# Optimization experiments

Hardware: AMD Instinct MI355X
Metric: run time of the kernel (lower is better)

## Reference

```python
import jax, jax.numpy as jnp
import numpy as np
import math

D_MODEL = 1024
N_HEADS = 16
FFN_DIM = 4096
B, L = 8, 1024
LN_EPS = 1e-5


def setup_inputs() -> dict:
    key = jax.random.key(0)
    ks = jax.random.split(key, 16)
    s = 1.0 / math.sqrt(D_MODEL)
    sf = 1.0 / math.sqrt(FFN_DIM)
    # weights stored [in, out] (transposed vs torch nn.Linear)
    return {
        "x": jax.random.normal(ks[0], (B, L, D_MODEL), dtype=jnp.float32),
        "Wq": jax.random.normal(ks[1], (D_MODEL, D_MODEL), dtype=jnp.float32) * s,
        "bq": jnp.zeros((D_MODEL,), jnp.float32),
        "Wk": jax.random.normal(ks[2], (D_MODEL, D_MODEL), dtype=jnp.float32) * s,
        "bk": jnp.zeros((D_MODEL,), jnp.float32),
        "Wv": jax.random.normal(ks[3], (D_MODEL, D_MODEL), dtype=jnp.float32) * s,
        "bv": jnp.zeros((D_MODEL,), jnp.float32),
        "Wo": jax.random.normal(ks[4], (D_MODEL, D_MODEL), dtype=jnp.float32) * s,
        "bo": jnp.zeros((D_MODEL,), jnp.float32),
        "W1": jax.random.normal(ks[5], (D_MODEL, FFN_DIM), dtype=jnp.float32) * s,
        "b1": jnp.zeros((FFN_DIM,), jnp.float32),
        "W2": jax.random.normal(ks[6], (FFN_DIM, D_MODEL), dtype=jnp.float32) * sf,
        "b2": jnp.zeros((D_MODEL,), jnp.float32),
        "gamma": jnp.ones((D_MODEL,), jnp.float32),
        "beta": jnp.zeros((D_MODEL,), jnp.float32),
    }


def reference(x, Wq, bq, Wk, bk, Wv, bv, Wo, bo, W1, b1, W2, b2, gamma, beta):
    Bb, Ll, D = x.shape
    H = N_HEADS
    E = D // H
    scale = 1.0 / math.sqrt(E)
    # multi-head attention (dropout is identity in eval)
    q = (x @ Wq + bq).reshape(Bb, Ll, H, E)
    k = (x @ Wk + bk).reshape(Bb, Ll, H, E)
    v = (x @ Wv + bv).reshape(Bb, Ll, H, E)
    scores = jnp.einsum('blhe,bshe->bhls', q, k)  # [B,H,L,L]
    A = jax.nn.softmax(scale * scores, axis=-1)
    ctx = jnp.einsum('bhls,bshd->blhd', A, v).reshape(Bb, Ll, D)
    attn_out = ctx @ Wo + bo
    x = x + attn_out
    # FFN: conv1d kernel_size=1 == pointwise linear; exact (erf) GELU as in F.gelu
    h = jax.nn.gelu(x @ W1 + b1, approximate=False)
    x = x + (h @ W2 + b2)
    # LayerNorm
    mu = jnp.mean(x, axis=-1, keepdims=True)
    var = jnp.mean(jnp.square(x - mu), axis=-1, keepdims=True)
    out = (x - mu) * jax.lax.rsqrt(var + LN_EPS) * gamma + beta
    return out
```

## Files before the change

### kernel.cpp

```cpp
#include <hip/hip_runtime.h>
#include <cmath>

typedef __attribute__((ext_vector_type(8))) _Float16 half8;
typedef __attribute__((ext_vector_type(4))) _Float16 half4;
typedef __attribute__((ext_vector_type(4))) float f32x4;

__device__ __forceinline__ void glds16(const void* g, void* l) {
  __builtin_amdgcn_global_load_lds(
      (__attribute__((address_space(1))) const void*)g,
      (__attribute__((address_space(3))) void*)l, 16, 0, 0);
}

__device__ __forceinline__ float fast_erf(float x) {
  float ax = fabsf(x);
  float t = 1.0f / (1.0f + 0.3275911f * ax);
  float y = t * (0.254829592f +
            t * (-0.284496736f +
            t * (1.421413741f +
            t * (-1.453152027f + t * 1.061405429f))));
  float r = 1.0f - y * __expf(-ax * ax);
  return copysignf(r, x);
}

__global__ __launch_bounds__(256) void k_cvt(const float* __restrict__ in,
                                             _Float16* __restrict__ out) {
  int i = (blockIdx.x * 256 + threadIdx.x) * 8;
  const f32x4* p = (const f32x4*)(in + i);
  f32x4 a = p[0], b = p[1];
  half8 h;
  h[0] = (_Float16)a[0]; h[1] = (_Float16)a[1]; h[2] = (_Float16)a[2]; h[3] = (_Float16)a[3];
  h[4] = (_Float16)b[0]; h[5] = (_Float16)b[1]; h[6] = (_Float16)b[2]; h[7] = (_Float16)b[3];
  *(half8*)(out + i) = h;
}

__global__ __launch_bounds__(256) void k_wt(const float* __restrict__ W,
                                            _Float16* __restrict__ Wt, int K, int N) {
  __shared__ float t[32][33];
  int x = threadIdx.x & 31, y4 = (threadIdx.x >> 5) << 2;
  int n0 = blockIdx.x << 5, k0 = blockIdx.y << 5;
#pragma unroll
  for (int r = 0; r < 4; ++r) t[y4 + r][x] = W[(size_t)(k0 + y4 + r) * N + n0 + x];
  __syncthreads();
#pragma unroll
  for (int r = 0; r < 4; ++r) Wt[(size_t)(n0 + y4 + r) * K + k0 + x] = (_Float16)t[x][y4 + r];
}

__global__ void k_biascat(const float* __restrict__ a, const float* __restrict__ b,
                          const float* __restrict__ c, float* __restrict__ o) {
  int i = blockIdx.x * 256 + threadIdx.x;
  const float* s = i < 1024 ? a : (i < 2048 ? b : c);
  o[i] = s[i & 1023];
}

template <int BM, int EPI>
__global__ __launch_bounds__(512, 2) void k_gemm8(
    const _Float16* __restrict__ A, const _Float16* __restrict__ Bt,
    const float* __restrict__ bias, const float* __restrict__ res,
    float* __restrict__ outf, _Float16* __restrict__ outh, int M, int N, int K) {
  constexpr int MR = BM / 32;
  constexpr int MH2 = MR / 2;
  constexpr int AL = BM * 64;
  constexpr int BL = 256 * 64;
  constexpr int ABYTES = BM * 128;
  constexpr int BBYTES = 256 * 128;
  constexpr int AB2 = 2 * ABYTES;
  __shared__ _Float16 lds[2 * (AL + BL)];
  const char* ldsc = (const char*)lds;

  const int tid = threadIdx.x;
  const int lane = tid & 63;
  const int w = tid >> 6, wr = w >> 2, wc = w & 3;
  const int l15 = lane & 15, grp = lane >> 4;

  const int gx = gridDim.x;
  const int nwg = gx * gridDim.y;
  const int lid = blockIdx.y * gx + blockIdx.x;
  const int wid = (lid & 7) * (nwg >> 3) + (lid >> 3);
  const int m0 = (wid / gx) * BM, n0 = (wid % gx) * 256;

  const int m2 = (l15 >> 2) & 1, m01 = l15 & 3;
  const int chunk0 = (m2 << 2) | (grp ^ m01);
  const int aoff0 = wr * 2048 + l15 * 128 + chunk0 * 16;
  const int aoff1 = aoff0 ^ 64;
  const int boff0 = wc * 2048 + l15 * 128 + chunk0 * 16;
  const int boff1 = boff0 ^ 64;

  const int srow = tid >> 3;
  const int scs8 = ((tid & 7) ^ (srow & 7)) * 8;
  const int NK = K >> 6;

  f32x4 acc[MR][4] = {};
  half8 af[MH2][2], bf[2][2];

#define STG_A(J, MHH, KN)                                                      \
  _Pragma("unroll") for (int s = 0; s < BM / 128; ++s)                         \
      glds16(A + (size_t)(m0 + (MHH) * (BM / 2) + s * 64 + srow) * K +         \
                 (size_t)(KN)*64 + scs8,                                       \
             lds + (J)*AL + ((MHH) * (BM / 2) + s * 64) * 64 + tid * 8);
#define STG_B(J, NHH, KN)                                                      \
  _Pragma("unroll") for (int s = 0; s < 2; ++s)                                \
      glds16(Bt + (size_t)(n0 + (NHH)*128 + s * 64 + srow) * K +               \
                  (size_t)(KN)*64 + scs8,                                      \
             lds + 2 * AL + (J)*BL + ((NHH)*128 + s * 64) * 64 + tid * 8);

#define STG_ALL(J, KN)                                                         \
  STG_A(J, 0, KN) STG_B(J, 0, KN) STG_B(J, 1, KN) STG_A(J, 1, KN)

#define VM_A asm volatile("s_waitcnt vmcnt(8)" ::: "memory")
#define VM_B asm volatile("s_waitcnt vmcnt(4)" ::: "memory")
#define VM_NONE

#define PHASE(J, MHQ, NHQ, RA, RB, STGSTMT, VMSTMT)                            \
  {                                                                            \
    if constexpr (RA) {                                                        \
      _Pragma("unroll") for (int i = 0; i < MH2; ++i) {                        \
        af[i][0] = *(const half8*)(ldsc + (J)*ABYTES +                         \
                                   ((MHQ)*MH2 + i) * 4096 + aoff0);            \
        af[i][1] = *(const half8*)(ldsc + (J)*ABYTES +                         \
                                   ((MHQ)*MH2 + i) * 4096 + aoff1);            \
      }                                                                        \
    }                                                                          \
    if constexpr (RB) {                                                        \
      _Pragma("unroll") for (int n = 0; n < 2; ++n) {                          \
        bf[n][0] = *(const half8*)(ldsc + AB2 + (J)*BBYTES +                   \
                                   ((NHQ)*2 + n) * 8192 + boff0);              \
        bf[n][1] = *(const half8*)(ldsc + AB2 + (J)*BBYTES +                   \
                                   ((NHQ)*2 + n) * 8192 + boff1);              \
      }                                                                        \
    }                                                                          \
    STGSTMT;                                                                   \
    __builtin_amdgcn_s_barrier();                                              \
    asm volatile("s_waitcnt lgkmcnt(0)");                                      \
    __builtin_amdgcn_sched_barrier(0);                                         \
    __builtin_amdgcn_s_setprio(1);                                             \
    _Pragma("unroll") for (int ks = 0; ks < 2; ++ks)                           \
        _Pragma("unroll") for (int i = 0; i < MH2; ++i)                        \
            _Pragma("unroll") for (int n = 0; n < 2; ++n)                      \
                acc[(MHQ)*MH2 + i][(NHQ)*2 + n] =                              \
                    __builtin_amdgcn_mfma_f32_16x16x32_f16(                    \
                        af[i][ks], bf[n][ks], acc[(MHQ)*MH2 + i][(NHQ)*2 + n], \
                        0, 0, 0);                                              \
    __builtin_amdgcn_s_setprio(0);                                             \
    VMSTMT;                                                                    \
    __builtin_amdgcn_s_barrier();                                              \
  }

#define KTILE(J, KT)                                                           \
  {                                                                            \
    const int kn_ = ((KT) + 1 < NK) ? (KT) + 1 : (KT);                         \
    PHASE(J, 0, 0, true, true, STG_ALL(1 - (J), kn_), VM_A)                    \
    PHASE(J, 0, 1, false, true, , VM_NONE)                                     \
    PHASE(J, 1, 1, true, false, , VM_NONE)                                     \
    PHASE(J, 1, 0, false, true, , VM_B)                                        \
  }

  STG_ALL(0, 0)
  VM_B;
  __builtin_amdgcn_s_barrier();

#pragma unroll 1
  for (int kt = 0; kt < NK; kt += 2) {
    KTILE(0, kt)
    KTILE(1, kt + 1)
  }
  asm volatile("s_waitcnt vmcnt(0)" ::: "memory");
#undef KTILE
#undef PHASE
#undef VM_A
#undef VM_B
#undef VM_NONE
#undef STG_ALL
#undef STG_A
#undef STG_B

  float bcol[4];
#pragma unroll
  for (int n = 0; n < 4; ++n) bcol[n] = bias[n0 + (n * 4 + wc) * 16 + l15];
#pragma unroll
  for (int m = 0; m < MR; ++m) {
#pragma unroll
    for (int rr = 0; rr < 4; ++rr) {
      const size_t row = m0 + (m * 2 + wr) * 16 + grp * 4 + rr;
#pragma unroll
      for (int n = 0; n < 4; ++n) {
        const int col = n0 + (n * 4 + wc) * 16 + l15;
        float v = acc[m][n][rr] + bcol[n];
        const size_t idx = row * N + col;
        if (EPI == 0) {
          outh[idx] = (_Float16)v;
        } else if (EPI == 1) {
          float t2 = v + res[idx];
          outf[idx] = t2;
          outh[idx] = (_Float16)t2;
        } else if (EPI == 2) {
          float g = 0.5f * v * (1.0f + fast_erf(v * 0.70710678118654752f));
          outh[idx] = (_Float16)g;
        } else {
          outf[idx] = v + res[idx];
        }
      }
    }
  }
}

template <int EPI>
__global__ __launch_bounds__(512, 2) void k_gemmf(
    const _Float16* __restrict__ A, const _Float16* __restrict__ Bt,
    const float* __restrict__ bias, const float* __restrict__ res,
    float* __restrict__ outf, _Float16* __restrict__ outh, int M, int N, int K) {
  constexpr int AL = 256 * 64, BL = 128 * 64;
  constexpr int ABY = 32768, BBY = 16384, BBASE = 3 * ABY;
  __shared__ _Float16 lds[3 * (AL + BL)];
  const char* ldsc = (const char*)lds;

  const int tid = threadIdx.x;
  const int lane = tid & 63;
  const int w = tid >> 6, wr = w >> 1, wc = w & 1;
  const int l15 = lane & 15, grp = lane >> 4;

  const int gx = gridDim.x;
  const int nwg = gx * gridDim.y;
  const int lid = blockIdx.y * gx + blockIdx.x;
  const int wid = (lid & 7) * (nwg >> 3) + (lid >> 3);
  const int m0 = (wid / gx) * 256, n0 = (wid % gx) * 128;

  const int m2 = (l15 >> 2) & 1, m01 = l15 & 3;
  const int c0 = ((m2 << 2) | (grp ^ m01)) * 16;
  const int aoff0 = wr * 2048 + l15 * 128 + c0;
  const int aoff1 = aoff0 ^ 64;
  const int boff0 = wc * 2048 + l15 * 128 + c0;
  const int boff1 = boff0 ^ 64;

  const int srow = tid >> 3;
  const int scs8 = ((tid & 7) ^ (srow & 7)) * 8;
  const int NK = K >> 6;

  const _Float16* aG = A + (size_t)(m0 + srow) * K + scs8;
  const _Float16* bG = Bt + (size_t)(n0 + srow) * K + scs8;

  f32x4 acc[4][4] = {};

#define FSTG_A(JJ, HH, KN)                                                     \
  _Pragma("unroll") for (int s = 0; s < 2; ++s)                                \
      glds16(aG + (size_t)((HH)*128 + s * 64) * K + (size_t)(KN)*64,           \
             lds + (JJ)*AL + ((HH)*128 + s * 64) * 64 + tid * 8);
#define FSTG_B(JJ, HH, KN)                                                     \
  glds16(bG + (size_t)((HH)*64) * K + (size_t)(KN)*64,                         \
         lds + 3 * AL + (JJ)*BL + (HH)*64 * 64 + tid * 8);

#define FPHASE(PA, PB, AO, BO, STGSTMT, VMSTMT)                                \
  {                                                                            \
    half8 af_[4], bf_[4];                                                      \
    _Pragma("unroll") for (int m = 0; m < 4; ++m)                              \
        af_[m] = *(const half8*)((PA) + m * 8192 + (AO));                      \
    _Pragma("unroll") for (int n = 0; n < 4; ++n)                              \
        bf_[n] = *(const half8*)((PB) + n * 4096 + (BO));                      \
    STGSTMT;                                                                   \
    __builtin_amdgcn_s_barrier();                                              \
    asm volatile("s_waitcnt lgkmcnt(0)");                                      \
    __builtin_amdgcn_sched_barrier(0);                                         \
    __builtin_amdgcn_s_setprio(1);                                             \
    _Pragma("unroll") for (int m = 0; m < 4; ++m)                              \
        _Pragma("unroll") for (int n = 0; n < 4; ++n)                          \
            acc[m][n] = __builtin_amdgcn_mfma_f32_16x16x32_f16(                \
                af_[m], bf_[n], acc[m][n], 0, 0, 0);                           \
    __builtin_amdgcn_s_setprio(0);                                             \
    VMSTMT;                                                                    \
    __builtin_amdgcn_s_barrier();                                              \
  }

  FSTG_A(0, 0, 0) FSTG_A(0, 1, 0) FSTG_B(0, 0, 0) FSTG_B(0, 1, 0)
  FSTG_A(1, 0, 1) FSTG_A(1, 1, 1) FSTG_B(1, 0, 1) FSTG_B(1, 1, 1)
  asm volatile("s_waitcnt vmcnt(6)" ::: "memory");
  __builtin_amdgcn_s_barrier();

  int j = 0, j2 = 2;
#pragma unroll 1
  for (int kt = 0; kt < NK; ++kt) {
    const int kn = (kt + 2 < NK) ? kt + 2 : NK - 1;
    const char* pa = ldsc + j * ABY;
    const char* pb = ldsc + BBASE + j * BBY;
    FPHASE(pa, pb, aoff0, boff0, { FSTG_A(j2, 0, kn) FSTG_B(j2, 0, kn) }, )
    FPHASE(pa, pb, aoff1, boff1, { FSTG_A(j2, 1, kn) FSTG_B(j2, 1, kn) },
           asm volatile("s_waitcnt vmcnt(6)" ::: "memory");)
    j = (j == 2) ? 0 : j + 1;
    j2 = (j2 == 2) ? 0 : j2 + 1;
  }
  asm volatile("s_waitcnt vmcnt(0)" ::: "memory");
#undef FPHASE
#undef FSTG_A
#undef FSTG_B

  float bcol[4];
#pragma unroll
  for (int n = 0; n < 4; ++n) bcol[n] = bias[n0 + (n * 2 + wc) * 16 + l15];
#pragma unroll
  for (int m = 0; m < 4; ++m) {
#pragma unroll
    for (int rr = 0; rr < 4; ++rr) {
      const size_t row = m0 + (m * 4 + wr) * 16 + grp * 4 + rr;
#pragma unroll
      for (int n = 0; n < 4; ++n) {
        const int col = n0 + (n * 2 + wc) * 16 + l15;
        float v = acc[m][n][rr] + bcol[n];
        const size_t idx = row * N + col;
        if (EPI == 0) {
          outh[idx] = (_Float16)v;
        } else if (EPI == 1) {
          float t2 = v + res[idx];
          outf[idx] = t2;
          outh[idx] = (_Float16)t2;
        } else if (EPI == 2) {
          float g = 0.5f * v * (1.0f + fast_erf(v * 0.70710678118654752f));
          outh[idx] = (_Float16)g;
        } else {
          outf[idx] = v + res[idx];
        }
      }
    }
  }
}

__global__ __launch_bounds__(256) void k_vt(const _Float16* __restrict__ qkv,
                                            _Float16* __restrict__ Vt) {
  __shared__ _Float16 t[64 * 66];
  const int tid = threadIdx.x;
  const int bh = blockIdx.y, b = bh >> 4, h = bh & 15;
  const int s0 = blockIdx.x << 6;
#pragma unroll
  for (int p = 0; p < 2; ++p) {
    int lin = p * 256 + tid;
    int s = lin >> 3, c8 = lin & 7;
    half8 v = *(const half8*)&qkv[(size_t)(b * 1024 + s0 + s) * 3072 + 2048 + h * 64 + c8 * 8];
    union { half8 h8; unsigned u[4]; } u;
    u.h8 = v;
    unsigned* d = (unsigned*)&t[s * 66 + c8 * 8];
#pragma unroll
    for (int k = 0; k < 4; ++k) d[k] = u.u[k];
  }
  __syncthreads();
#pragma unroll
  for (int p = 0; p < 2; ++p) {
    int lin = p * 256 + tid;
    int e = lin >> 3, c8 = lin & 7;
    half8 v;
#pragma unroll
    for (int j = 0; j < 8; ++j) v[j] = t[(c8 * 8 + j) * 66 + e];
    *(half8*)&Vt[(size_t)(bh * 64 + e) * 1024 + s0 + c8 * 8] = v;
  }
}

__global__ __launch_bounds__(256) void k_attn(const _Float16* __restrict__ qkv,
                                              const _Float16* __restrict__ Vt,
                                              _Float16* __restrict__ ctx) {
  __shared__ _Float16 Ks[128 * 64];
  __shared__ _Float16 Vs[64 * 128];
  __shared__ _Float16 Ps[4][16 * 136];
  const int tid = threadIdx.x;
  const int lane = tid & 63, w = tid >> 6;
  const int l15 = lane & 15, grp = lane >> 4;
  const int bh = blockIdx.y, b = bh >> 4, h = bh & 15;
  const int q0 = blockIdx.x << 6;
  const float CSC = 0.125f * 1.44269504088896f;

  half8 qf[2];
  {
    const _Float16* qp = qkv + (size_t)(b * 1024 + q0 + w * 16 + l15) * 3072 + h * 64 + grp * 8;
    qf[0] = *(const half8*)qp;
    qf[1] = *(const half8*)(qp + 32);
  }
  f32x4 octx[4] = {};
  float mrun = -1e30f, lrun = 0.f;

  for (int kt = 0; kt < 8; ++kt) {
    const int s0 = kt * 128;
#pragma unroll
    for (int i = 0; i < 4; ++i) {
      {
        int srow = i * 32 + (tid >> 3);
        int c8 = (tid & 7) ^ (srow & 7);
        glds16(qkv + (size_t)(b * 1024 + s0 + srow) * 3072 + 1024 + h * 64 + c8 * 8,
               Ks + w * 512 + i * 2048);
      }
      {
        int erow = i * 16 + (tid >> 4);
        int c16 = (tid & 15) ^ (erow & 7);
        glds16(Vt + (size_t)(bh * 64 + erow) * 1024 + s0 + c16 * 8,
               Vs + w * 512 + i * 2048);
      }
    }
    __syncthreads();
    f32x4 sacc[8] = {};
#pragma unroll
    for (int ks = 0; ks < 2; ++ks)
#pragma unroll
      for (int f = 0; f < 8; ++f) {
        int srow = f * 16 + l15;
        half8 kf = *(const half8*)&Ks[srow * 64 + ((ks * 32 + grp * 8) ^ ((srow & 7) * 8))];
        sacc[f] = __builtin_amdgcn_mfma_f32_16x16x32_f16(kf, qf[ks], sacc[f], 0, 0, 0);
      }
    float sv[8][4];
    float tmax = -1e30f;
#pragma unroll
    for (int f = 0; f < 8; ++f)
#pragma unroll
      for (int r = 0; r < 4; ++r) {
        float v = sacc[f][r] * CSC;
        sv[f][r] = v;
        tmax = fmaxf(tmax, v);
      }
    tmax = fmaxf(tmax, __shfl_xor(tmax, 16));
    tmax = fmaxf(tmax, __shfl_xor(tmax, 32));
    float mnew = fmaxf(mrun, tmax);
    float corr = exp2f(mrun - mnew);
    float tsum = 0.f;
#pragma unroll
    for (int f = 0; f < 8; ++f)
#pragma unroll
      for (int r = 0; r < 4; ++r) {
        float pv = exp2f(sv[f][r] - mnew);
        sv[f][r] = pv;
        tsum += pv;
      }
    tsum += __shfl_xor(tsum, 16);
    tsum += __shfl_xor(tsum, 32);
    lrun = lrun * corr + tsum;
    mrun = mnew;
#pragma unroll
    for (int r = 0; r < 4; ++r) {
      float cq = __shfl(corr, (lane & 48) + grp * 4 + r);
#pragma unroll
      for (int jf = 0; jf < 4; ++jf) octx[jf][r] *= cq;
    }
#pragma unroll
    for (int f = 0; f < 8; ++f) {
      half4 pk;
      pk[0] = (_Float16)sv[f][0]; pk[1] = (_Float16)sv[f][1];
      pk[2] = (_Float16)sv[f][2]; pk[3] = (_Float16)sv[f][3];
      *(half4*)&Ps[w][l15 * 136 + f * 16 + grp * 4] = pk;
    }
#pragma unroll
    for (int ks2 = 0; ks2 < 4; ++ks2) {
      half8 pa = *(const half8*)&Ps[w][l15 * 136 + ks2 * 32 + grp * 8];
#pragma unroll
      for (int jf = 0; jf < 4; ++jf) {
        int erow = jf * 16 + l15;
        half8 vb = *(const half8*)&Vs[erow * 128 + ((ks2 * 32 + grp * 8) ^ ((erow & 7) * 8))];
        octx[jf] = __builtin_amdgcn_mfma_f32_16x16x32_f16(pa, vb, octx[jf], 0, 0, 0);
      }
    }
    __syncthreads();
  }
#pragma unroll
  for (int r = 0; r < 4; ++r) {
    float lq = __shfl(lrun, (lane & 48) + grp * 4 + r);
    float inv = 1.0f / lq;
    const size_t row = b * 1024 + q0 + w * 16 + grp * 4 + r;
#pragma unroll
    for (int jf = 0; jf < 4; ++jf)
      ctx[row * 1024 + h * 64 + jf * 16 + l15] = (_Float16)(octx[jf][r] * inv);
  }
}

__global__ __launch_bounds__(256) void k_ln(const float* xin, const float* __restrict__ gamma,
                                            const float* __restrict__ beta, float* out) {
  __shared__ float red[8];
  const int tid = threadIdx.x;
  const size_t row = blockIdx.x;
  f32x4 v = *(const f32x4*)&xin[row * 1024 + tid * 4];
  float s = v[0] + v[1] + v[2] + v[3];
  float s2 = v[0] * v[0] + v[1] * v[1] + v[2] * v[2] + v[3] * v[3];
#pragma unroll
  for (int o = 32; o >= 1; o >>= 1) {
    s += __shfl_xor(s, o);
    s2 += __shfl_xor(s2, o);
  }
  if ((tid & 63) == 0) { red[tid >> 6] = s; red[4 + (tid >> 6)] = s2; }
  __syncthreads();
  s = red[0] + red[1] + red[2] + red[3];
  s2 = red[4] + red[5] + red[6] + red[7];
  float mu = s * (1.0f / 1024.0f);
  float var = s2 * (1.0f / 1024.0f) - mu * mu;
  float rs = rsqrtf(var + 1e-5f);
  f32x4 g = *(const f32x4*)&gamma[tid * 4];
  f32x4 bt = *(const f32x4*)&beta[tid * 4];
  f32x4 o4;
#pragma unroll
  for (int r = 0; r < 4; ++r) o4[r] = (v[r] - mu) * rs * g[r] + bt[r];
  *(f32x4*)&out[row * 1024 + tid * 4] = o4;
}

extern "C" void kernel_launch(void* const* d_in, const int* in_sizes, int n_in,
                              void* d_out, int out_size, void* d_ws, size_t ws_size,
                              hipStream_t stream) {
  (void)in_sizes; (void)n_in; (void)out_size; (void)ws_size;
  const float* x  = (const float*)d_in[0];
  const float* Wq = (const float*)d_in[1];  const float* bq = (const float*)d_in[2];
  const float* Wk = (const float*)d_in[3];  const float* bk = (const float*)d_in[4];
  const float* Wv = (const float*)d_in[5];  const float* bv = (const float*)d_in[6];
  const float* Wo = (const float*)d_in[7];  const float* bo = (const float*)d_in[8];
  const float* W1 = (const float*)d_in[9];  const float* b1 = (const float*)d_in[10];
  const float* W2 = (const float*)d_in[11]; const float* b2 = (const float*)d_in[12];
  const float* gamma = (const float*)d_in[13];
  const float* beta  = (const float*)d_in[14];
  float* out = (float*)d_out;

  char* p = (char*)d_ws;
  _Float16* xb    = (_Float16*)p;  p += (size_t)16 << 20;
  _Float16* qkv   = (_Float16*)p;
  _Float16* hbuf  = (_Float16*)p;  p += (size_t)48 << 20;
  _Float16* Vt    = (_Float16*)p;  p += (size_t)16 << 20;
  _Float16* Wqkvt = (_Float16*)p;  p += (size_t)3072 * 1024 * 2;
  _Float16* Wot   = (_Float16*)p;  p += (size_t)1024 * 1024 * 2;
  _Float16* W1t   = (_Float16*)p;  p += (size_t)4096 * 1024 * 2;
  _Float16* W2t   = (_Float16*)p;  p += (size_t)4096 * 1024 * 2;
  float*    bqkv  = (float*)p;     p += (size_t)3072 * 4;
  float*    x1    = (float*)p;     p += (size_t)32 << 20;
  _Float16* x1b   = (_Float16*)p;  p += (size_t)16 << 20;
  _Float16* ctx   = xb;

  k_cvt<<<4096, 256, 0, stream>>>(x, xb);
  k_wt<<<dim3(32, 32), 256, 0, stream>>>(Wq, Wqkvt, 1024, 1024);
  k_wt<<<dim3(32, 32), 256, 0, stream>>>(Wk, Wqkvt + 1024 * 1024, 1024, 1024);
  k_wt<<<dim3(32, 32), 256, 0, stream>>>(Wv, Wqkvt + 2048 * 1024, 1024, 1024);
  k_wt<<<dim3(32, 32), 256, 0, stream>>>(Wo, Wot, 1024, 1024);
  k_wt<<<dim3(128, 32), 256, 0, stream>>>(W1, W1t, 1024, 4096);
  k_wt<<<dim3(32, 128), 256, 0, stream>>>(W2, W2t, 4096, 1024);
  k_biascat<<<12, 256, 0, stream>>>(bq, bk, bv, bqkv);

  k_gemmf<0><<<dim3(24, 32), 512, 0, stream>>>(xb, Wqkvt, bqkv, nullptr, nullptr, qkv,
                                               8192, 3072, 1024);
  k_vt<<<dim3(16, 128), 256, 0, stream>>>(qkv, Vt);
  k_attn<<<dim3(16, 128), 256, 0, stream>>>(qkv, Vt, ctx);
  k_gemmf<1><<<dim3(8, 32), 512, 0, stream>>>(ctx, Wot, bo, x, x1, x1b, 8192, 1024, 1024);
  k_gemm8<256, 2><<<dim3(16, 32), 512, 0, stream>>>(x1b, W1t, b1, nullptr, nullptr, hbuf,
                                                    8192, 4096, 1024);
  k_gemmf<3><<<dim3(8, 32), 512, 0, stream>>>(hbuf, W2t, b2, x1, out, nullptr,
                                              8192, 1024, 4096);
  k_ln<<<8192, 256, 0, stream>>>(out, gamma, beta, out);
}
```

Baseline: 373.0 us.

## Spread k_gemm8 prefetch across phases and drop the fp32 residual buffer

The k_gemm8 main loop now issues its next-tile global-to-LDS loads one piece per compute phase, and one B half is prefetched two tiles ahead. A single vmcnt(2) wait replaces the two earlier waits. The aim is to smooth memory traffic and hide latency better. Separately, the Wo GEMM no longer writes the fp32 residual x1, and the final GEMM reads the fp16 copy x1b as the residual. This removes a 32 MB write and cuts the residual read in half, at the cost of precision in the residual path.

After: 360.3 us. -3.4%, faster.

```diff
diff --git a/kernel.cpp b/kernel.cpp
--- a/kernel.cpp
+++ b/kernel.cpp
@@ -103,11 +103,7 @@
                   (size_t)(KN)*64 + scs8,                                      \
              lds + 2 * AL + (J)*BL + ((NHH)*128 + s * 64) * 64 + tid * 8);
 
-#define STG_ALL(J, KN)                                                         \
-  STG_A(J, 0, KN) STG_B(J, 0, KN) STG_B(J, 1, KN) STG_A(J, 1, KN)
-
-#define VM_A asm volatile("s_waitcnt vmcnt(8)" ::: "memory")
-#define VM_B asm volatile("s_waitcnt vmcnt(4)" ::: "memory")
+#define VM_C asm volatile("s_waitcnt vmcnt(2)" ::: "memory")
 #define VM_NONE
 
 #define PHASE(J, MHQ, NHQ, RA, RB, STGSTMT, VMSTMT)                            \
@@ -147,15 +143,17 @@
 
 #define KTILE(J, KT)                                                           \
   {                                                                            \
-    const int kn_ = ((KT) + 1 < NK) ? (KT) + 1 : (KT);                         \
-    PHASE(J, 0, 0, true, true, STG_ALL(1 - (J), kn_), VM_A)                    \
-    PHASE(J, 0, 1, false, true, , VM_NONE)                                     \
-    PHASE(J, 1, 1, true, false, , VM_NONE)                                     \
-    PHASE(J, 1, 0, false, true, , VM_B)                                        \
-  }
-
-  STG_ALL(0, 0)
-  VM_B;
+    const int kn_ = ((KT) + 1 < NK) ? (KT) + 1 : NK - 1;                       \
+    const int kn2_ = ((KT) + 2 < NK) ? (KT) + 2 : NK - 1;                      \
+    PHASE(J, 0, 0, true, true, STG_A(1 - (J), 0, kn_), VM_NONE)                \
+    PHASE(J, 0, 1, false, true, STG_A(1 - (J), 1, kn_), VM_NONE)               \
+    PHASE(J, 1, 1, true, false, STG_B(1 - (J), 0, kn_), VM_NONE)               \
+    PHASE(J, 1, 0, false, true, STG_B(J, 1, kn2_), VM_C)                       \
+  }
+
+  STG_A(0, 0, 0) STG_A(0, 1, 0) STG_B(0, 0, 0) STG_B(0, 1, 0)
+  STG_B(1, 1, 1)
+  VM_C;
   __builtin_amdgcn_s_barrier();
 
 #pragma unroll 1
@@ -166,10 +164,8 @@
   asm volatile("s_waitcnt vmcnt(0)" ::: "memory");
 #undef KTILE
 #undef PHASE
-#undef VM_A
-#undef VM_B
+#undef VM_C
 #undef VM_NONE
-#undef STG_ALL
 #undef STG_A
 #undef STG_B
 
@@ -206,7 +202,7 @@
 template <int EPI>
 __global__ __launch_bounds__(512, 2) void k_gemmf(
     const _Float16* __restrict__ A, const _Float16* __restrict__ Bt,
-    const float* __restrict__ bias, const float* __restrict__ res,
+    const float* __restrict__ bias, const void* __restrict__ res,
     float* __restrict__ outf, _Float16* __restrict__ outh, int M, int N, int K) {
   constexpr int AL = 256 * 64, BL = 128 * 64;
   constexpr int ABY = 32768, BBY = 16384, BBASE = 3 * ABY;
@@ -307,14 +303,14 @@
         if (EPI == 0) {
           outh[idx] = (_Float16)v;
         } else if (EPI == 1) {
-          float t2 = v + res[idx];
-          outf[idx] = t2;
+          float t2 = v + ((const float*)res)[idx];
           outh[idx] = (_Float16)t2;
         } else if (EPI == 2) {
           float g = 0.5f * v * (1.0f + fast_erf(v * 0.70710678118654752f));
           outh[idx] = (_Float16)g;
         } else {
-          outf[idx] = v + res[idx];
+          float t2 = v + (float)((const _Float16*)res)[idx];
+          outf[idx] = t2;
         }
       }
     }
@@ -515,7 +511,6 @@
   _Float16* W1t   = (_Float16*)p;  p += (size_t)4096 * 1024 * 2;
   _Float16* W2t   = (_Float16*)p;  p += (size_t)4096 * 1024 * 2;
   float*    bqkv  = (float*)p;     p += (size_t)3072 * 4;
-  float*    x1    = (float*)p;     p += (size_t)32 << 20;
   _Float16* x1b   = (_Float16*)p;  p += (size_t)16 << 20;
   _Float16* ctx   = xb;
 
@@ -532,10 +527,11 @@
                                                8192, 3072, 1024);
   k_vt<<<dim3(16, 128), 256, 0, stream>>>(qkv, Vt);
   k_attn<<<dim3(16, 128), 256, 0, stream>>>(qkv, Vt, ctx);
-  k_gemmf<1><<<dim3(8, 32), 512, 0, stream>>>(ctx, Wot, bo, x, x1, x1b, 8192, 1024, 1024);
+  k_gemmf<1><<<dim3(8, 32), 512, 0, stream>>>(ctx, Wot, bo, x, nullptr, x1b,
+                                              8192, 1024, 1024);
   k_gemm8<256, 2><<<dim3(16, 32), 512, 0, stream>>>(x1b, W1t, b1, nullptr, nullptr, hbuf,
                                                     8192, 4096, 1024);
-  k_gemmf<3><<<dim3(8, 32), 512, 0, stream>>>(hbuf, W2t, b2, x1, out, nullptr,
+  k_gemmf<4><<<dim3(8, 32), 512, 0, stream>>>(hbuf, W2t, b2, x1b, out, nullptr,
                                               8192, 1024, 4096);
   k_ln<<<8192, 256, 0, stream>>>(out, gamma, beta, out);
 }
```
